# Optimization experiments

Measured on AMD Instinct MI355X. Metric: run time of the kernel, lower is better.

The kernel has to match this reference:

```python
import jax, jax.numpy as jnp
import numpy as np

N_NODES = 100000
K_HOPS = 2


def _add_self_loops(edge_index, n):
    loop = jnp.arange(n, dtype=edge_index.dtype)
    src = jnp.concatenate([edge_index[0], loop])
    dst = jnp.concatenate([edge_index[1], loop])
    return src, dst


def _gcn_norm(src, dst, n):
    # symmetric normalization D^-1/2 (A+I) D^-1/2
    deg = jax.ops.segment_sum(jnp.ones_like(dst, dtype=jnp.float32), dst, num_segments=n)
    dinv = jnp.where(deg > 0, jax.lax.rsqrt(deg), 0.0)
    return dinv[src] * dinv[dst]  # [E]


def setup_inputs() -> dict:
    key = jax.random.key(0)
    k1, k2, k3, k4, k5 = jax.random.split(key, 5)
    in_f, out_f = 128, 64
    x = jax.random.normal(k1, (N_NODES, in_f), dtype=jnp.float32)
    edge_index = jax.random.randint(k2, (2, 1600000), 0, N_NODES, dtype=jnp.int64)
    s1 = 1.0 / np.sqrt(in_f)
    W1 = jax.random.uniform(k3, (in_f, in_f), dtype=jnp.float32, minval=-s1, maxval=s1)
    b1 = jnp.zeros((in_f,), dtype=jnp.float32)
    W2 = jax.random.uniform(k4, (out_f, in_f), dtype=jnp.float32, minval=-s1, maxval=s1)
    b2 = jnp.zeros((out_f,), dtype=jnp.float32)
    return {"x": x, "edge_index": edge_index, "W1": W1, "b1": b1, "W2": W2, "b2": b2}


def reference(x, edge_index, W1, b1, W2, b2):
    n = x.shape[0]
    src, dst = _add_self_loops(edge_index, n)
    norm = _gcn_norm(src, dst, n)
    for _ in range(K_HOPS):
        msg = x[src] * norm[:, None]                      # [E+N, F] gather
        x = jax.ops.segment_sum(msg, dst, num_segments=n)  # scatter-add
    # transform: Linear -> ReLU -> Linear -> log_softmax
    h = jax.nn.relu(x @ W1.T + b1)
    logits = h @ W2.T + b2
    return jax.nn.log_softmax(logits, axis=1)
```

## Files before the change

kernel.cpp:

```cpp
#include <hip/hip_runtime.h>
#include <math.h>

#define CAP 64
#define NSLICE 8

typedef __attribute__((ext_vector_type(8))) short short8;
typedef __attribute__((ext_vector_type(4))) float f32x4;
typedef __attribute__((ext_vector_type(4))) int int4v;

static __device__ inline unsigned short f2bf(float f) {
    unsigned int u = __float_as_uint(f);
    u += 0x7fffu + ((u >> 16) & 1u);
    return (unsigned short)(u >> 16);
}
static __device__ inline float bf_lo(unsigned int u) { return __uint_as_float(u << 16); }
static __device__ inline float bf_hi(unsigned int u) { return __uint_as_float(u & 0xffff0000u); }
static __device__ inline unsigned int pack2(float lo, float hi) {
    return ((unsigned int)f2bf(hi) << 16) | (unsigned int)f2bf(lo);
}


__global__ __launch_bounds__(256) void fill_swz_k(
    const int* __restrict__ dst, const int* __restrict__ src, int E,
    int sl, int n, int* __restrict__ cnt, int* __restrict__ bkt)
{
    int s  = blockIdx.x & (NSLICE - 1);
    int g  = blockIdx.x >> 3;
    int ng = gridDim.x >> 3;
    int lo = s * sl;
    int hi = lo + sl < n ? lo + sl : n;

    int stride = ng * 256 * 4;
    for (int base = (g * 256 + threadIdx.x) * 4; base < E; base += stride) {
        if (base + 4 <= E) {
            int4v d4 = __builtin_nontemporal_load((const int4v*)(dst + base));
#pragma unroll
            for (int j = 0; j < 4; j++) {
                int d = d4[j];
                if (d >= lo && d < hi) {
                    int sv = __builtin_nontemporal_load(src + base + j);
                    int pos = atomicAdd(&cnt[d], 1);
                    if (pos < CAP) bkt[(size_t)d * CAP + pos] = sv;
                }
            }
        } else {
            for (int e = base; e < E; e++) {
                int d = dst[e];
                if (d >= lo && d < hi) {
                    int pos = atomicAdd(&cnt[d], 1);
                    if (pos < CAP) bkt[(size_t)d * CAP + pos] = src[e];
                }
            }
        }
    }
}

__global__ void dinv_k(const int* __restrict__ cnt, float* __restrict__ dinv, int n) {
    int v = blockIdx.x * blockDim.x + threadIdx.x;
    if (v < n) dinv[v] = rsqrtf((float)(cnt[v] + 1));
}


__global__ void conv_x_k(const float2* __restrict__ x, const float* __restrict__ dinv,
                         unsigned int* __restrict__ xb, int n) {
    int i = blockIdx.x * blockDim.x + threadIdx.x;
    if (i < n * 64) {
        float sc = dinv[i >> 6];
        float2 v = x[i];
        xb[i] = pack2(v.x * sc, v.y * sc);
    }
}

__global__ void conv_w_k(const float2* __restrict__ in, unsigned int* __restrict__ out, int n2) {
    int i = blockIdx.x * blockDim.x + threadIdx.x;
    if (i < n2) {
        float2 v = in[i];
        out[i] = pack2(v.x, v.y);
    }
}


template<bool SQ>
__global__ __launch_bounds__(256) void gather_b_k(
    const unsigned int* __restrict__ xin,
    const int* __restrict__ cnt, const int* __restrict__ bkt,
    const float* __restrict__ dinv,
    unsigned int* __restrict__ xout, int n)
{
    int v = blockIdx.x * 4 + (threadIdx.x >> 6);
    if (v >= n) return;
    int l = threadIdx.x & 63;
    int c = cnt[v]; if (c > CAP) c = CAP;
    const int* __restrict__ b = bkt + (size_t)v * CAP;

    unsigned int us = xin[(size_t)v * 64 + l];
    float ax = 0.f, ay = 0.f;

    for (int i = 0; i < c; i += 8) {
        int4v b0 = *(const int4v*)(b + i);
        int4v b1 = *(const int4v*)(b + i + 4);
        int idx[8];
#pragma unroll
        for (int j = 0; j < 4; j++) idx[j]     = (i + j     < c) ? b0[j] : v;
#pragma unroll
        for (int j = 0; j < 4; j++) idx[4 + j] = (i + 4 + j < c) ? b1[j] : v;
        unsigned int u[8];
#pragma unroll
        for (int j = 0; j < 8; j++) u[j] = xin[(size_t)idx[j] * 64 + l];
#pragma unroll
        for (int j = 0; j < 8; j++) {
            if (i + j < c) { ax += bf_lo(u[j]); ay += bf_hi(u[j]); }
        }
    }

    ax += bf_lo(us);
    ay += bf_hi(us);

    float dv = dinv[v];
    float sc = SQ ? dv * dv : dv;
    xout[(size_t)v * 64 + l] = pack2(ax * sc, ay * sc);
}

__global__ __launch_bounds__(256) void transform_mfma_k(
    const unsigned short* __restrict__ x2b,
    const unsigned short* __restrict__ w1b,
    const float* __restrict__ b1,
    const unsigned short* __restrict__ w2b,
    const float* __restrict__ b2,
    float* __restrict__ out, int n)
{
    __shared__ __align__(16) unsigned short Hs[64][152];

    int t = threadIdx.x;
    int w = t >> 6;
    int l = t & 63;
    int lg = l >> 4;
    int ll = l & 15;
    int node0 = blockIdx.x * 64;

    int nrow = node0 + w * 16 + ll;
    int crow = nrow < n ? nrow : (n - 1);
    const unsigned short* xrow = x2b + (size_t)crow * 128 + lg * 8;
    short8 a[4];
#pragma unroll
    for (int kb = 0; kb < 4; kb++)
        a[kb] = *(const short8*)(xrow + kb * 32);

    f32x4 acc[8];
#pragma unroll
    for (int nt = 0; nt < 8; nt++) {
        float bv = b1[nt * 16 + ll];
        acc[nt][0] = bv; acc[nt][1] = bv; acc[nt][2] = bv; acc[nt][3] = bv;
    }
#pragma unroll
    for (int nt = 0; nt < 8; nt++) {
        const unsigned short* wrow = w1b + (size_t)(nt * 16 + ll) * 128 + lg * 8;
#pragma unroll
        for (int kb = 0; kb < 4; kb++) {
            short8 bf = *(const short8*)(wrow + kb * 32);
            acc[nt] = __builtin_amdgcn_mfma_f32_16x16x32_bf16(a[kb], bf, acc[nt], 0, 0, 0);
        }
    }

#pragma unroll
    for (int nt = 0; nt < 8; nt++) {
#pragma unroll
        for (int r = 0; r < 4; r++) {
            float hv = fmaxf(acc[nt][r], 0.f);
            Hs[w * 16 + lg * 4 + r][nt * 16 + ll] = f2bf(hv);
        }
    }

    short8 ha[4];
#pragma unroll
    for (int kb = 0; kb < 4; kb++)
        ha[kb] = *(const short8*)&Hs[w * 16 + ll][kb * 32 + lg * 8];

    f32x4 acc2[4];
#pragma unroll
    for (int nt = 0; nt < 4; nt++) {
        float bv = b2[nt * 16 + ll];
        acc2[nt][0] = bv; acc2[nt][1] = bv; acc2[nt][2] = bv; acc2[nt][3] = bv;
        const unsigned short* wrow = w2b + (size_t)(nt * 16 + ll) * 128 + lg * 8;
#pragma unroll
        for (int kb = 0; kb < 4; kb++) {
            short8 bf = *(const short8*)(wrow + kb * 32);
            acc2[nt] = __builtin_amdgcn_mfma_f32_16x16x32_bf16(ha[kb], bf, acc2[nt], 0, 0, 0);
        }
    }

#pragma unroll
    for (int r = 0; r < 4; r++) {
        float m = fmaxf(fmaxf(acc2[0][r], acc2[1][r]), fmaxf(acc2[2][r], acc2[3][r]));
        m = fmaxf(m, __shfl_xor(m, 1));
        m = fmaxf(m, __shfl_xor(m, 2));
        m = fmaxf(m, __shfl_xor(m, 4));
        m = fmaxf(m, __shfl_xor(m, 8));
        float s = __expf(acc2[0][r] - m) + __expf(acc2[1][r] - m) +
                  __expf(acc2[2][r] - m) + __expf(acc2[3][r] - m);
        s += __shfl_xor(s, 1);
        s += __shfl_xor(s, 2);
        s += __shfl_xor(s, 4);
        s += __shfl_xor(s, 8);
        float lse = m + __logf(s);
        int node = node0 + w * 16 + lg * 4 + r;
        if (node < n) {
#pragma unroll
            for (int nt = 0; nt < 4; nt++)
                out[(size_t)node * 64 + nt * 16 + ll] = acc2[nt][r] - lse;
        }
    }
}


static inline size_t align256(size_t x) { return (x + 255) & ~(size_t)255; }

extern "C" void kernel_launch(void* const* d_in, const int* in_sizes, int n_in,
                              void* d_out, int out_size, void* d_ws, size_t ws_size,
                              hipStream_t stream) {
    const float* x  = (const float*)d_in[0];
    const int*   ei = (const int*)d_in[1];
    const float* W1 = (const float*)d_in[2];
    const float* b1 = (const float*)d_in[3];
    const float* W2 = (const float*)d_in[4];
    const float* b2 = (const float*)d_in[5];
    float* out = (float*)d_out;

    int n = in_sizes[0] / 128;
    int E = in_sizes[1] / 2;
    const int* src = ei;
    const int* dst = ei + E;

    char* w = (char*)d_ws;
    size_t off = 0;
    int*          cnt  = (int*)(w + off);          off += align256((size_t)n * sizeof(int));
    float*        dinv = (float*)(w + off);        off += align256((size_t)n * sizeof(float));
    int*          bkt  = (int*)(w + off);          off += align256((size_t)n * CAP * sizeof(int));
    unsigned int* xb   = (unsigned int*)(w + off); off += align256((size_t)n * 64 * sizeof(unsigned int));
    unsigned int* z1b  = (unsigned int*)(w + off); off += align256((size_t)n * 64 * sizeof(unsigned int));
    unsigned int* x2b  = (unsigned int*)(w + off); off += align256((size_t)n * 64 * sizeof(unsigned int));
    unsigned int* w1b  = (unsigned int*)(w + off); off += align256((size_t)128 * 64 * sizeof(unsigned int));
    unsigned int* w2b  = (unsigned int*)(w + off);

    int tb = 256;
    int gb_n = (n + tb - 1) / tb;
    int gb_x = (n * 64 + tb - 1) / tb;
    int gb_g = (n + 3) / 4;

    (void)hipMemsetAsync(cnt, 0, (size_t)n * sizeof(int), stream);
    int sl = (n + NSLICE - 1) / NSLICE;
    fill_swz_k<<<2048, tb, 0, stream>>>(dst, src, E, sl, n, cnt, bkt);
    dinv_k<<<gb_n, tb, 0, stream>>>(cnt, dinv, n);

    conv_x_k<<<gb_x, tb, 0, stream>>>((const float2*)x, dinv, xb, n);
    conv_w_k<<<(128 * 64 + tb - 1) / tb, tb, 0, stream>>>((const float2*)W1, w1b, 128 * 64);
    conv_w_k<<<(64 * 64 + tb - 1) / tb, tb, 0, stream>>>((const float2*)W2, w2b, 64 * 64);

    gather_b_k<true ><<<gb_g, tb, 0, stream>>>(xb,  cnt, bkt, dinv, z1b, n);
    gather_b_k<false><<<gb_g, tb, 0, stream>>>(z1b, cnt, bkt, dinv, x2b, n);

    transform_mfma_k<<<(n + 63) / 64, 256, 0, stream>>>(
        (const unsigned short*)x2b, (const unsigned short*)w1b, b1,
        (const unsigned short*)w2b, b2, out, n);
}
```

Before: 275.3 us.

## Assign fill slices by hardware XCC id with dynamic per-slice work stealing

The bucket-fill kernel now picks its destination slice from the hardware XCC_ID register instead of blockIdx, so each slice's atomics and bucket writes stay in one XCD's L2. Blocks grab 2048-edge chunks from a per-slice atomic counter, so every slice covers the whole edge list no matter how blocks land on XCDs. This aims to cut cross-die atomic traffic and balance the load. It adds per-chunk atomics and barriers, and it relies on the number of XCDs matching NSLICE; if some XCC id has no resident blocks, that slice's edges would be dropped.

Result: slower. 338.2 us (+22.9%).

```diff
diff --git a/kernel.cpp b/kernel.cpp
--- a/kernel.cpp
+++ b/kernel.cpp
@@ -3,6 +3,7 @@
 
 #define CAP 64
 #define NSLICE 8
+#define FCHUNK 2048
 
 typedef __attribute__((ext_vector_type(8))) short short8;
 typedef __attribute__((ext_vector_type(4))) float f32x4;
@@ -18,33 +19,54 @@
 static __device__ inline unsigned int pack2(float lo, float hi) {
     return ((unsigned int)f2bf(hi) << 16) | (unsigned int)f2bf(lo);
 }
-
-
-__global__ __launch_bounds__(256) void fill_swz_k(
+static __device__ inline int xcc_id() {
+    unsigned v;
+    asm volatile("s_getreg_b32 %0, hwreg(HW_REG_XCC_ID)" : "=s"(v));
+    return (int)(v & (NSLICE - 1));
+}
+
+
+__global__ __launch_bounds__(256) void fill_xcd_k(
     const int* __restrict__ dst, const int* __restrict__ src, int E,
-    int sl, int n, int* __restrict__ cnt, int* __restrict__ bkt)
+    int sl, int n, int* __restrict__ cnt, int* __restrict__ bkt,
+    int* __restrict__ work)
 {
-    int s  = blockIdx.x & (NSLICE - 1);
-    int g  = blockIdx.x >> 3;
-    int ng = gridDim.x >> 3;
+    int s  = xcc_id();
     int lo = s * sl;
     int hi = lo + sl < n ? lo + sl : n;
-
-    int stride = ng * 256 * 4;
-    for (int base = (g * 256 + threadIdx.x) * 4; base < E; base += stride) {
-        if (base + 4 <= E) {
-            int4v d4 = __builtin_nontemporal_load((const int4v*)(dst + base));
+    __shared__ int sbase;
+
+    for (;;) {
+        if (threadIdx.x == 0) sbase = atomicAdd(&work[s], FCHUNK);
+        __syncthreads();
+        int base = sbase;
+        __syncthreads();
+        if (base >= E) break;
+
+        int e0 = base + threadIdx.x * 8;
+        if (e0 + 8 <= E) {
+            int4v d4a = __builtin_nontemporal_load((const int4v*)(dst + e0));
+            int4v d4b = __builtin_nontemporal_load((const int4v*)(dst + e0 + 4));
 #pragma unroll
             for (int j = 0; j < 4; j++) {
-                int d = d4[j];
+                int d = d4a[j];
                 if (d >= lo && d < hi) {
-                    int sv = __builtin_nontemporal_load(src + base + j);
+                    int sv = __builtin_nontemporal_load(src + e0 + j);
+                    int pos = atomicAdd(&cnt[d], 1);
+                    if (pos < CAP) bkt[(size_t)d * CAP + pos] = sv;
+                }
+            }
+#pragma unroll
+            for (int j = 0; j < 4; j++) {
+                int d = d4b[j];
+                if (d >= lo && d < hi) {
+                    int sv = __builtin_nontemporal_load(src + e0 + 4 + j);
                     int pos = atomicAdd(&cnt[d], 1);
                     if (pos < CAP) bkt[(size_t)d * CAP + pos] = sv;
                 }
             }
         } else {
-            for (int e = base; e < E; e++) {
+            for (int e = e0; e < E; e++) {
                 int d = dst[e];
                 if (d >= lo && d < hi) {
                     int pos = atomicAdd(&cnt[d], 1);
@@ -234,6 +256,7 @@
     char* w = (char*)d_ws;
     size_t off = 0;
     int*          cnt  = (int*)(w + off);          off += align256((size_t)n * sizeof(int));
+    int*          work = (int*)(w + off);          off += 256;
     float*        dinv = (float*)(w + off);        off += align256((size_t)n * sizeof(float));
     int*          bkt  = (int*)(w + off);          off += align256((size_t)n * CAP * sizeof(int));
     unsigned int* xb   = (unsigned int*)(w + off); off += align256((size_t)n * 64 * sizeof(unsigned int));
@@ -248,8 +271,9 @@
     int gb_g = (n + 3) / 4;
 
     (void)hipMemsetAsync(cnt, 0, (size_t)n * sizeof(int), stream);
+    (void)hipMemsetAsync(work, 0, 256, stream);
     int sl = (n + NSLICE - 1) / NSLICE;
-    fill_swz_k<<<2048, tb, 0, stream>>>(dst, src, E, sl, n, cnt, bkt);
+    fill_xcd_k<<<2048, tb, 0, stream>>>(dst, src, E, sl, n, cnt, bkt, work);
     dinv_k<<<gb_n, tb, 0, stream>>>(cnt, dinv, n);
 
     conv_x_k<<<gb_x, tb, 0, stream>>>((const float2*)x, dinv, xb, n);
```

## Partition edges into per-slice queues before bucket scatter

Applied to the files above, without the earlier changes.

Replaces the slice-filtered bucket fill, where each of eight slice groups rescanned the whole dst array, with two passes. The first partitions edges once into eight slice queues using LDS counters and one global atomic per slice per block. The second scatters each queue into the per-node buckets so the atomics stay localized per slice. This cuts the repeated reads of the edge list. In exchange it writes and rereads an intermediate queue (aliased onto the xb buffer) and adds a kernel launch. The queue capacity QCAP must hold each slice's edge count.

Result: slower. 284.1 us (+3.2%).

```diff
diff --git a/kernel.cpp b/kernel.cpp
--- a/kernel.cpp
+++ b/kernel.cpp
@@ -3,6 +3,7 @@
 
 #define CAP 64
 #define NSLICE 8
+#define QCAP 400000
 
 typedef __attribute__((ext_vector_type(8))) short short8;
 typedef __attribute__((ext_vector_type(4))) float f32x4;
@@ -20,38 +21,67 @@
 }
 
 
-__global__ __launch_bounds__(256) void fill_swz_k(
+__global__ __launch_bounds__(256) void part_k(
     const int* __restrict__ dst, const int* __restrict__ src, int E,
-    int sl, int n, int* __restrict__ cnt, int* __restrict__ bkt)
+    unsigned long long mul, int2* __restrict__ queue, int* __restrict__ qcnt)
 {
-    int s  = blockIdx.x & (NSLICE - 1);
-    int g  = blockIdx.x >> 3;
-    int ng = gridDim.x >> 3;
-    int lo = s * sl;
-    int hi = lo + sl < n ? lo + sl : n;
-
-    int stride = ng * 256 * 4;
-    for (int base = (g * 256 + threadIdx.x) * 4; base < E; base += stride) {
-        if (base + 4 <= E) {
-            int4v d4 = __builtin_nontemporal_load((const int4v*)(dst + base));
-#pragma unroll
-            for (int j = 0; j < 4; j++) {
-                int d = d4[j];
-                if (d >= lo && d < hi) {
-                    int sv = __builtin_nontemporal_load(src + base + j);
-                    int pos = atomicAdd(&cnt[d], 1);
-                    if (pos < CAP) bkt[(size_t)d * CAP + pos] = sv;
-                }
-            }
-        } else {
-            for (int e = base; e < E; e++) {
-                int d = dst[e];
-                if (d >= lo && d < hi) {
-                    int pos = atomicAdd(&cnt[d], 1);
-                    if (pos < CAP) bkt[(size_t)d * CAP + pos] = src[e];
-                }
-            }
-        }
+    __shared__ int lcnt[NSLICE];
+    __shared__ int gbase[NSLICE];
+    if (threadIdx.x < NSLICE) lcnt[threadIdx.x] = 0;
+    __syncthreads();
+
+    int base = blockIdx.x * 2048 + threadIdx.x * 8;
+    int nv = E - base; nv = nv > 8 ? 8 : (nv < 0 ? 0 : nv);
+
+    int d[8], sv[8], sl[8], lp[8];
+    if (nv == 8) {
+        int4v da = __builtin_nontemporal_load((const int4v*)(dst + base));
+        int4v db = __builtin_nontemporal_load((const int4v*)(dst + base + 4));
+        int4v sa = __builtin_nontemporal_load((const int4v*)(src + base));
+        int4v sb = __builtin_nontemporal_load((const int4v*)(src + base + 4));
+#pragma unroll
+        for (int j = 0; j < 4; j++) {
+            d[j] = da[j]; sv[j] = sa[j];
+            d[4 + j] = db[j]; sv[4 + j] = sb[j];
+        }
+    } else {
+        for (int j = 0; j < nv; j++) { d[j] = dst[base + j]; sv[j] = src[base + j]; }
+    }
+
+#pragma unroll
+    for (int j = 0; j < 8; j++) {
+        if (j < nv) {
+            sl[j] = (int)(((unsigned long long)(unsigned)d[j] * mul) >> 40);
+            lp[j] = atomicAdd(&lcnt[sl[j]], 1);
+        }
+    }
+    __syncthreads();
+    if (threadIdx.x < NSLICE)
+        gbase[threadIdx.x] = atomicAdd(&qcnt[threadIdx.x], lcnt[threadIdx.x]);
+    __syncthreads();
+#pragma unroll
+    for (int j = 0; j < 8; j++) {
+        if (j < nv) {
+            int p = gbase[sl[j]] + lp[j];
+            if (p < QCAP) queue[(size_t)sl[j] * QCAP + p] = make_int2(d[j], sv[j]);
+        }
+    }
+}
+
+
+__global__ __launch_bounds__(256) void scat_k(
+    const int2* __restrict__ queue, const int* __restrict__ qcnt,
+    int* __restrict__ cnt, int* __restrict__ bkt)
+{
+    int s = blockIdx.x & (NSLICE - 1);
+    int m = qcnt[s]; if (m > QCAP) m = QCAP;
+    int i0 = (blockIdx.x >> 3) * 256 + threadIdx.x;
+    int stride = (gridDim.x >> 3) * 256;
+    const int2* __restrict__ q = queue + (size_t)s * QCAP;
+    for (int i = i0; i < m; i += stride) {
+        int2 r = q[i];
+        int pos = atomicAdd(&cnt[r.x], 1);
+        if (pos < CAP) bkt[(size_t)r.x * CAP + pos] = r.y;
     }
 }
 
@@ -234,6 +264,7 @@
     char* w = (char*)d_ws;
     size_t off = 0;
     int*          cnt  = (int*)(w + off);          off += align256((size_t)n * sizeof(int));
+    int*          qcnt = (int*)(w + off);          off += 256;
     float*        dinv = (float*)(w + off);        off += align256((size_t)n * sizeof(float));
     int*          bkt  = (int*)(w + off);          off += align256((size_t)n * CAP * sizeof(int));
     unsigned int* xb   = (unsigned int*)(w + off); off += align256((size_t)n * 64 * sizeof(unsigned int));
@@ -241,15 +272,21 @@
     unsigned int* x2b  = (unsigned int*)(w + off); off += align256((size_t)n * 64 * sizeof(unsigned int));
     unsigned int* w1b  = (unsigned int*)(w + off); off += align256((size_t)128 * 64 * sizeof(unsigned int));
     unsigned int* w2b  = (unsigned int*)(w + off);
+    int2* queue = (int2*)xb;
 
     int tb = 256;
     int gb_n = (n + tb - 1) / tb;
     int gb_x = (n * 64 + tb - 1) / tb;
     int gb_g = (n + 3) / 4;
+    int gb_p = (E + 2047) / 2048;
+
+    int sl = (n + NSLICE - 1) / NSLICE;
+    unsigned long long mul = ((1ULL << 40) + (unsigned long long)sl - 1) / (unsigned long long)sl;
 
     (void)hipMemsetAsync(cnt, 0, (size_t)n * sizeof(int), stream);
-    int sl = (n + NSLICE - 1) / NSLICE;
-    fill_swz_k<<<2048, tb, 0, stream>>>(dst, src, E, sl, n, cnt, bkt);
+    (void)hipMemsetAsync(qcnt, 0, NSLICE * sizeof(int), stream);
+    part_k<<<gb_p, tb, 0, stream>>>(dst, src, E, mul, queue, qcnt);
+    scat_k<<<2048, tb, 0, stream>>>(queue, qcnt, cnt, bkt);
     dinv_k<<<gb_n, tb, 0, stream>>>(cnt, dinv, n);
 
     conv_x_k<<<gb_x, tb, 0, stream>>>((const float2*)x, dinv, xb, n);
```
